# Optimization experiments

Measured on AMD Instinct MI355X. Metric: run time of the kernel, lower is better.

The kernel has to match this reference:

```python
import jax, jax.numpy as jnp
import numpy as np

N, E, F0, HEADS, B, OUT = 100000, 1600000, 128, 4, 64, 32
CHANNELS = [16, 8, 4, 2]
NEG_SLOPE = 0.2


def setup_inputs() -> dict:
    key = jax.random.key(0)
    ks = jax.random.split(key, 40)
    inp = {}
    inp['x'] = jax.random.normal(ks[0], (N, F0), dtype=jnp.float32)
    inp['edge_index'] = jax.random.randint(ks[1], (2, E), 0, N, dtype=jnp.int64)
    inp['batch'] = jnp.sort(jax.random.randint(ks[2], (N,), 0, B, dtype=jnp.int64))
    # GATConv params per layer: W [in, heads*out], att_src/att_dst [heads, out], bias [heads*out]
    in_dim = F0
    ki = 3
    for li, oc in enumerate(CHANNELS, start=1):
        scale = 1.0 / np.sqrt(in_dim)
        inp[f'W{li}'] = jax.random.normal(ks[ki], (in_dim, HEADS * oc), dtype=jnp.float32) * scale
        inp[f'a_src{li}'] = jax.random.normal(ks[ki + 1], (HEADS, oc), dtype=jnp.float32) * 0.1
        inp[f'a_dst{li}'] = jax.random.normal(ks[ki + 2], (HEADS, oc), dtype=jnp.float32) * 0.1
        inp[f'b{li}'] = jnp.zeros((HEADS * oc,), dtype=jnp.float32)
        ki += 3
        in_dim = HEADS * oc
    inp['W_fc'] = jax.random.normal(ks[ki], (2 * HEADS, OUT), dtype=jnp.float32) * (1.0 / np.sqrt(2 * HEADS))
    inp['b_fc'] = jnp.zeros((OUT,), dtype=jnp.float32)
    return inp


def gat_layer(x, src, dst, W, a_src, a_dst, b, oc):
    n = x.shape[0]
    h = (x @ W).reshape(n, HEADS, oc)                    # [N, H, C]
    al_s = jnp.einsum('nhc,hc->nh', h, a_src)            # [N, H]
    al_d = jnp.einsum('nhc,hc->nh', h, a_dst)
    e = jax.nn.leaky_relu(al_s[src] + al_d[dst], NEG_SLOPE)  # [E, H]
    # segment softmax over incoming edges per destination node
    m = jax.ops.segment_max(e, dst, num_segments=n)
    m = jnp.where(jnp.isfinite(m), m, 0.0)
    ex = jnp.exp(e - m[dst])
    s = jax.ops.segment_sum(ex, dst, num_segments=n)
    alpha = ex / (s[dst] + 1e-16)                        # [E, H]
    out = jax.ops.segment_sum(h[src] * alpha[:, :, None], dst, num_segments=n)
    return out.reshape(n, HEADS * oc) + b


def reference(x, edge_index, batch, W1, a_src1, a_dst1, b1, W2, a_src2, a_dst2, b2,
              W3, a_src3, a_dst3, b3, W4, a_src4, a_dst4, b4, W_fc, b_fc):
    n = x.shape[0]
    loops = jnp.arange(n, dtype=edge_index.dtype)
    src = jnp.concatenate([edge_index[0], loops])   # PyG GATConv adds self-loops
    dst = jnp.concatenate([edge_index[1], loops])
    params = [(W1, a_src1, a_dst1, b1), (W2, a_src2, a_dst2, b2),
              (W3, a_src3, a_dst3, b3), (W4, a_src4, a_dst4, b4)]
    h = x
    for (W, a_s, a_d, b), oc in zip(params, CHANNELS):
        h = jax.nn.relu(gat_layer(h, src, dst, W, a_s, a_d, b, oc))
        # dropout(0.3) is identity at inference
    # global mean pool over graphs in the batch
    sums = jax.ops.segment_sum(h, batch, num_segments=B)
    cnt = jax.ops.segment_sum(jnp.ones((n,), h.dtype), batch, num_segments=B)
    pooled = sums / jnp.maximum(cnt, 1.0)[:, None]
    return pooled @ W_fc + b_fc
```

## Files before the change

### kernel.cpp

```cpp
#include <hip/hip_runtime.h>
#include <hip/hip_bf16.h>

#define NNODES 100000
#define NEDGES 1600000
#define NHEADS 4
#define NGRAPH 64
#define NOUTF  32
#define BSH    9
#define NBUK   ((NNODES + 511) >> 9)
#define BPAD   16
#define BCAP   9216
#define CGRID  512
#define ECAP   ((NEDGES + CGRID - 1) / CGRID)
#define G1GRID ((NNODES + 63) / 64)

__device__ __forceinline__ unsigned short f2bf(float f) {
    union { float f; unsigned u; } v;
    v.f = f;
    unsigned r = v.u + 0x7FFF + ((v.u >> 16) & 1);
    return (unsigned short)(r >> 16);
}
__device__ __forceinline__ float bflo(unsigned u) {
    union { unsigned u; float f; } v;
    v.u = u << 16;
    return v.f;
}
__device__ __forceinline__ float bfhi(unsigned u) {
    union { unsigned u; float f; } v;
    v.u = u & 0xFFFF0000u;
    return v.f;
}

__device__ __forceinline__ bool ei_is_int64(const int* __restrict__ ei) {
    int acc = 0;
    #pragma unroll
    for (int i = 0; i < 32; i++) acc |= ei[2 * i + 1];
    return acc == 0;
}

__device__ __forceinline__ void fma4(float4& a, float s, const float4& b) {
    a.x += s * b.x;
    a.y += s * b.y;
    a.z += s * b.z;
    a.w += s * b.w;
}

__global__ __launch_bounds__(256) void gat_coarse_gemm1_kernel(
        const int* __restrict__ ei, const int* __restrict__ bt,
        int* __restrict__ bkcur, int* __restrict__ packed, int* __restrict__ bat,
        const float* __restrict__ x, const float* __restrict__ W1,
        const float* __restrict__ as1, const float* __restrict__ ad1,
        unsigned short* __restrict__ h1, float* __restrict__ al_s,
        float* __restrict__ al_d, int ne, int n) {
    __shared__ float smem[64 * 64 + 64 * 132];
    const int tid = threadIdx.x;
    if (blockIdx.x < CGRID) {
        int* hist = (int*)smem;
        int* base = hist + 256;
        int* es = base + 256;
        int* ed = es + ECAP;
        for (int i = tid; i < NBUK; i += 256) hist[i] = 0;
        __syncthreads();
        bool wide = ei_is_int64(ei);
        int chunk = (ne + CGRID - 1) / CGRID;
        int e0 = blockIdx.x * chunk;
        int e1 = min(e0 + chunk, ne);
        for (int i = e0 + tid; i < e1; i += 256) {
            int s = wide ? ei[2 * i] : ei[i];
            int d = wide ? ei[2 * (ne + i)] : ei[ne + i];
            es[i - e0] = s;
            ed[i - e0] = d;
            atomicAdd(&hist[d >> BSH], 1);
        }
        __syncthreads();
        for (int i = tid; i < NBUK; i += 256)
            base[i] = hist[i] ? atomicAdd(&bkcur[i * BPAD], hist[i]) : 0;
        __syncthreads();
        for (int i = tid; i < NBUK; i += 256) hist[i] = 0;
        __syncthreads();
        int m = e1 - e0;
        for (int j = tid; j < m; j += 256) {
            int d = ed[j];
            int bk = d >> BSH;
            int pos = base[bk] + atomicAdd(&hist[bk], 1);
            if (pos < BCAP) packed[bk * BCAP + pos] = es[j] | ((d & 511) << 17);
        }
        int gid = blockIdx.x * 256 + tid;
        for (int i = gid; i < n; i += CGRID * 256) bat[i] = wide ? bt[2 * i] : bt[i];
    } else {
        constexpr int DIN = 128, DOUT = 64, KTILE = 64;
        constexpr int OG = DOUT / 4;
        constexpr int NPB = 64;
        constexpr int S = DIN + 4;
        constexpr int C = DOUT / NHEADS;
        float* Wl = smem;
        float* xs = smem + KTILE * DOUT;
        const int base = (blockIdx.x - CGRID) * NPB;
        constexpr int KC = DIN / 4;
        for (int i = tid; i < NPB * KC; i += 256) {
            int nn = i / KC, kc = i - nn * KC;
            int nd = base + nn;
            float4 v = (nd < n) ? ((const float4*)x)[(size_t)nd * KC + kc]
                                : make_float4(0.f, 0.f, 0.f, 0.f);
            *(float4*)&xs[nn * S + kc * 4] = v;
        }
        const int og = tid % OG;
        const int ng = tid / OG;
        const int n0 = ng * 4;
        float4 acc[4] = {};
        for (int kt = 0; kt < DIN; kt += KTILE) {
            __syncthreads();
            for (int i = tid; i < KTILE * OG; i += 256)
                ((float4*)Wl)[i] = ((const float4*)W1)[kt * OG + i];
            __syncthreads();
            #pragma unroll 2
            for (int k = 0; k < KTILE; k += 4) {
                float4 wv[4], xv[4];
                #pragma unroll
                for (int j = 0; j < 4; j++)
                    wv[j] = *(const float4*)&Wl[(k + j) * DOUT + og * 4];
                #pragma unroll
                for (int r = 0; r < 4; r++)
                    xv[r] = *(const float4*)&xs[(n0 + r) * S + kt + k];
                #pragma unroll
                for (int r = 0; r < 4; r++) {
                    fma4(acc[r], xv[r].x, wv[0]);
                    fma4(acc[r], xv[r].y, wv[1]);
                    fma4(acc[r], xv[r].z, wv[2]);
                    fma4(acc[r], xv[r].w, wv[3]);
                }
            }
        }
        float4 asv = ((const float4*)as1)[og];
        float4 adv = ((const float4*)ad1)[og];
        #pragma unroll
        for (int r = 0; r < 4; r++) {
            int node = base + n0 + r;
            bool ok = node < n;
            if (ok) {
                ushort4 o;
                o.x = f2bf(acc[r].x);
                o.y = f2bf(acc[r].y);
                o.z = f2bf(acc[r].z);
                o.w = f2bf(acc[r].w);
                ((ushort4*)h1)[(size_t)node * OG + og] = o;
            }
            float ps = acc[r].x * asv.x + acc[r].y * asv.y + acc[r].z * asv.z + acc[r].w * asv.w;
            float pd = acc[r].x * adv.x + acc[r].y * adv.y + acc[r].z * adv.z + acc[r].w * adv.w;
            #pragma unroll
            for (int off = 1; off < C / 4; off <<= 1) {
                ps += __shfl_xor(ps, off);
                pd += __shfl_xor(pd, off);
            }
            if (ok && (og % (C / 4)) == 0) {
                int hh = og / (C / 4);
                al_s[node * NHEADS + hh] = ps;
                al_d[node * NHEADS + hh] = pd;
            }
        }
    }
}

__global__ __launch_bounds__(1024) void gat_fine_kernel(
        const int* __restrict__ packed, const int* __restrict__ bkcur,
        int* __restrict__ row_ptr, int* __restrict__ col, int n) {
    __shared__ int bscan[256];
    __shared__ int dg[512];
    __shared__ int excl[512];
    __shared__ int partial[256];
    __shared__ int cur[512];
    int b = blockIdx.x;
    int tid = threadIdx.x;
    if (tid < 256) bscan[tid] = (tid < NBUK) ? bkcur[tid * BPAD] : 0;
    if (tid < 512) dg[tid] = 0;
    __syncthreads();
    for (int off = 1; off < 256; off <<= 1) {
        int u = (tid < 256 && tid >= off) ? bscan[tid - off] : 0;
        __syncthreads();
        if (tid < 256) bscan[tid] += u;
        __syncthreads();
    }
    int cntb = bkcur[b * BPAD];
    int csr0 = bscan[b] - cntb;
    int pbeg = b * BCAP;
    int pend = pbeg + cntb;
    for (int t = pbeg + tid; t < pend; t += 1024)
        atomicAdd(&dg[packed[t] >> 17], 1);
    __syncthreads();
    int a0 = 0, a1 = 0, s = 0;
    if (tid < 256) {
        a0 = dg[2 * tid];
        a1 = dg[2 * tid + 1];
        s = a0 + a1;
        partial[tid] = s;
    }
    __syncthreads();
    for (int off = 1; off < 256; off <<= 1) {
        int u = (tid < 256 && tid >= off) ? partial[tid - off] : 0;
        __syncthreads();
        if (tid < 256) partial[tid] += u;
        __syncthreads();
    }
    if (tid < 256) {
        int ebase = partial[tid] - s;
        excl[2 * tid] = ebase;
        excl[2 * tid + 1] = ebase + a0;
        cur[2 * tid] = ebase;
        cur[2 * tid + 1] = ebase + a0;
    }
    __syncthreads();
    int node0 = b << BSH;
    if (tid < 512) {
        int nd = node0 + tid;
        if (nd < n) row_ptr[nd] = csr0 + excl[tid];
    }
    if (b == NBUK - 1 && tid == 0) row_ptr[n] = bscan[NBUK - 1];
    for (int t = pbeg + tid; t < pend; t += 1024) {
        int v = packed[t];
        int pos = atomicAdd(&cur[v >> 17], 1);
        col[csr0 + pos] = v & 0x1FFFF;
    }
}

__global__ __launch_bounds__(256) void gat_agg1_gemm2_kernel(
        const unsigned short* __restrict__ h, const float* __restrict__ al_s,
        const float* __restrict__ al_d_l1, const int* __restrict__ row_ptr,
        const int* __restrict__ col, const float* __restrict__ b1,
        const float* __restrict__ W2, const float* __restrict__ as2,
        const float* __restrict__ ad2, char* __restrict__ hrow_out,
        float* __restrict__ al_d, int n) {
    __shared__ float Wl[64 * 32];
    __shared__ float xs[32 * 68];
    const int tid = threadIdx.x;
    for (int i = tid; i < 64 * 32 / 4; i += 256)
        ((float4*)Wl)[i] = ((const float4*)W2)[i];
    __syncthreads();
    int lane = tid & 63;
    int sub = lane & 7;
    int gidx = lane >> 3;
    int slot = (tid >> 6) * 8 + gidx;
    int node = blockIdx.x * 32 + slot;
    bool ok = node < n;
    int node_c = ok ? node : (n - 1);
    int beg = row_ptr[node_c];
    int cnt = row_ptr[node_c + 1] - beg;
    const uint4* h4 = (const uint4*)h;
    float acc[8] = {};
    int j0 = sub * 8;
    const int hh = sub >> 1;
    float ald = al_d_l1[node_c * NHEADS + hh];
    float ws = 0.f;
    int total = cnt + 1;
    int t = 0;
    for (; t + 2 <= total; t += 2) {
        int s0 = col[beg + t];
        int s1 = (t + 1 < cnt) ? col[beg + t + 1] : node_c;
        float e0 = al_s[s0 * NHEADS + hh] + ald;
        float e1 = al_s[s1 * NHEADS + hh] + ald;
        uint4 hv0 = h4[(size_t)s0 * 8 + sub];
        uint4 hv1 = h4[(size_t)s1 * 8 + sub];
        e0 = (e0 > 0.f) ? e0 : 0.2f * e0;
        e1 = (e1 > 0.f) ? e1 : 0.2f * e1;
        float w0 = __expf(e0);
        float w1 = __expf(e1);
        ws += w0;
        acc[0] += w0 * bflo(hv0.x);
        acc[1] += w0 * bfhi(hv0.x);
        acc[2] += w0 * bflo(hv0.y);
        acc[3] += w0 * bfhi(hv0.y);
        acc[4] += w0 * bflo(hv0.z);
        acc[5] += w0 * bfhi(hv0.z);
        acc[6] += w0 * bflo(hv0.w);
        acc[7] += w0 * bfhi(hv0.w);
        ws += w1;
        acc[0] += w1 * bflo(hv1.x);
        acc[1] += w1 * bfhi(hv1.x);
        acc[2] += w1 * bflo(hv1.y);
        acc[3] += w1 * bfhi(hv1.y);
        acc[4] += w1 * bflo(hv1.z);
        acc[5] += w1 * bfhi(hv1.z);
        acc[6] += w1 * bflo(hv1.w);
        acc[7] += w1 * bfhi(hv1.w);
    }
    if (t < total) {
        int s0 = (t < cnt) ? col[beg + t] : node_c;
        float e0 = al_s[s0 * NHEADS + hh] + ald;
        uint4 hv0 = h4[(size_t)s0 * 8 + sub];
        e0 = (e0 > 0.f) ? e0 : 0.2f * e0;
        float w0 = __expf(e0);
        ws += w0;
        acc[0] += w0 * bflo(hv0.x);
        acc[1] += w0 * bfhi(hv0.x);
        acc[2] += w0 * bflo(hv0.y);
        acc[3] += w0 * bfhi(hv0.y);
        acc[4] += w0 * bflo(hv0.z);
        acc[5] += w0 * bfhi(hv0.z);
        acc[6] += w0 * bflo(hv0.w);
        acc[7] += w0 * bfhi(hv0.w);
    }
    float inv = 1.f / (ws + 1e-16f);
    #pragma unroll
    for (int k = 0; k < 8; k++) {
        acc[k] = acc[k] * inv + b1[j0 + k];
        acc[k] = (acc[k] > 0.f) ? acc[k] : 0.f;
    }
    float* xrow = &xs[slot * 68];
    *(float4*)&xrow[j0] = make_float4(acc[0], acc[1], acc[2], acc[3]);
    *(float4*)&xrow[j0 + 4] = make_float4(acc[4], acc[5], acc[6], acc[7]);
    const float4* Wl4 = (const float4*)Wl;
    float4 out4 = make_float4(0.f, 0.f, 0.f, 0.f);
    #pragma unroll 4
    for (int k = 0; k < 64; k += 4) {
        float4 xv = *(const float4*)&xrow[k];
        float4 w0 = Wl4[(k + 0) * 8 + sub];
        float4 w1 = Wl4[(k + 1) * 8 + sub];
        float4 w2 = Wl4[(k + 2) * 8 + sub];
        float4 w3 = Wl4[(k + 3) * 8 + sub];
        fma4(out4, xv.x, w0);
        fma4(out4, xv.y, w1);
        fma4(out4, xv.z, w2);
        fma4(out4, xv.w, w3);
    }
    float4 asv = ((const float4*)as2)[sub];
    float4 adv = ((const float4*)ad2)[sub];
    char* rp = hrow_out + (size_t)node_c * 96;
    if (ok) {
        ushort4 o;
        o.x = f2bf(out4.x);
        o.y = f2bf(out4.y);
        o.z = f2bf(out4.z);
        o.w = f2bf(out4.w);
        *(ushort4*)(rp + 16 + 8 * sub) = o;
    }
    float ps = out4.x * asv.x + out4.y * asv.y + out4.z * asv.z + out4.w * asv.w;
    float pd = out4.x * adv.x + out4.y * adv.y + out4.z * adv.z + out4.w * adv.w;
    ps += __shfl_xor(ps, 1);
    pd += __shfl_xor(pd, 1);
    if (ok && (sub & 1) == 0) {
        int hh2 = sub >> 1;
        *(float*)(rp + 4 * hh2) = ps;
        al_d[node_c * NHEADS + hh2] = pd;
    }
}

__global__ __launch_bounds__(256) void gat_agg2_gemm3_kernel(
        const char* __restrict__ hrow, const float* __restrict__ al_d_in,
        const int* __restrict__ row_ptr, const int* __restrict__ col,
        const float* __restrict__ b2, const float* __restrict__ W3,
        const float* __restrict__ as3, const float* __restrict__ ad3,
        char* __restrict__ hrow_out, float* __restrict__ al_d, int n) {
    __shared__ float Wl[32 * 16];
    __shared__ float xs[64 * 36];
    const int tid = threadIdx.x;
    for (int i = tid; i < 32 * 16 / 4; i += 256)
        ((float4*)Wl)[i] = ((const float4*)W3)[i];
    __syncthreads();
    int lane = tid & 63;
    int sub = lane & 3;
    int gidx = lane >> 2;
    int slot = (tid >> 6) * 16 + gidx;
    int node = blockIdx.x * 64 + slot;
    bool ok = node < n;
    int node_c = ok ? node : (n - 1);
    int beg = row_ptr[node_c];
    int cnt = row_ptr[node_c + 1] - beg;
    float acc[8] = {};
    int j0 = sub * 8;
    const int hh = sub;
    float ald = al_d_in[node_c * NHEADS + hh];
    float ws = 0.f;
    int total = cnt + 1;
    int t = 0;
    for (; t + 2 <= total; t += 2) {
        int s0 = col[beg + t];
        int s1 = (t + 1 < cnt) ? col[beg + t + 1] : node_c;
        const char* r0 = hrow + (size_t)s0 * 96;
        const char* r1 = hrow + (size_t)s1 * 96;
        float e0 = *(const float*)(r0 + 4 * hh) + ald;
        float e1 = *(const float*)(r1 + 4 * hh) + ald;
        uint4 hv0 = *(const uint4*)(r0 + 16 + 16 * sub);
        uint4 hv1 = *(const uint4*)(r1 + 16 + 16 * sub);
        e0 = (e0 > 0.f) ? e0 : 0.2f * e0;
        e1 = (e1 > 0.f) ? e1 : 0.2f * e1;
        float w0 = __expf(e0);
        float w1 = __expf(e1);
        ws += w0;
        acc[0] += w0 * bflo(hv0.x);
        acc[1] += w0 * bfhi(hv0.x);
        acc[2] += w0 * bflo(hv0.y);
        acc[3] += w0 * bfhi(hv0.y);
        acc[4] += w0 * bflo(hv0.z);
        acc[5] += w0 * bfhi(hv0.z);
        acc[6] += w0 * bflo(hv0.w);
        acc[7] += w0 * bfhi(hv0.w);
        ws += w1;
        acc[0] += w1 * bflo(hv1.x);
        acc[1] += w1 * bfhi(hv1.x);
        acc[2] += w1 * bflo(hv1.y);
        acc[3] += w1 * bfhi(hv1.y);
        acc[4] += w1 * bflo(hv1.z);
        acc[5] += w1 * bfhi(hv1.z);
        acc[6] += w1 * bflo(hv1.w);
        acc[7] += w1 * bfhi(hv1.w);
    }
    if (t < total) {
        int s0 = (t < cnt) ? col[beg + t] : node_c;
        const char* r0 = hrow + (size_t)s0 * 96;
        float e0 = *(const float*)(r0 + 4 * hh) + ald;
        uint4 hv0 = *(const uint4*)(r0 + 16 + 16 * sub);
        e0 = (e0 > 0.f) ? e0 : 0.2f * e0;
        float w0 = __expf(e0);
        ws += w0;
        acc[0] += w0 * bflo(hv0.x);
        acc[1] += w0 * bfhi(hv0.x);
        acc[2] += w0 * bflo(hv0.y);
        acc[3] += w0 * bfhi(hv0.y);
        acc[4] += w0 * bflo(hv0.z);
        acc[5] += w0 * bfhi(hv0.z);
        acc[6] += w0 * bflo(hv0.w);
        acc[7] += w0 * bfhi(hv0.w);
    }
    float inv = 1.f / (ws + 1e-16f);
    #pragma unroll
    for (int k = 0; k < 8; k++) {
        acc[k] = acc[k] * inv + b2[j0 + k];
        acc[k] = (acc[k] > 0.f) ? acc[k] : 0.f;
    }
    float* xrow = &xs[slot * 36];
    *(float4*)&xrow[j0] = make_float4(acc[0], acc[1], acc[2], acc[3]);
    *(float4*)&xrow[j0 + 4] = make_float4(acc[4], acc[5], acc[6], acc[7]);
    const float4* Wl4 = (const float4*)Wl;
    float4 out4 = make_float4(0.f, 0.f, 0.f, 0.f);
    #pragma unroll 4
    for (int k = 0; k < 32; k += 4) {
        float4 xv = *(const float4*)&xrow[k];
        float4 w0 = Wl4[(k + 0) * 4 + sub];
        float4 w1 = Wl4[(k + 1) * 4 + sub];
        float4 w2 = Wl4[(k + 2) * 4 + sub];
        float4 w3 = Wl4[(k + 3) * 4 + sub];
        fma4(out4, xv.x, w0);
        fma4(out4, xv.y, w1);
        fma4(out4, xv.z, w2);
        fma4(out4, xv.w, w3);
    }
    float4 asv = ((const float4*)as3)[sub];
    float4 adv = ((const float4*)ad3)[sub];
    char* rp = hrow_out + (size_t)node_c * 64;
    if (ok) {
        ushort4 o;
        o.x = f2bf(out4.x);
        o.y = f2bf(out4.y);
        o.z = f2bf(out4.z);
        o.w = f2bf(out4.w);
        *(ushort4*)(rp + 16 + 8 * sub) = o;
        float ps = out4.x * asv.x + out4.y * asv.y + out4.z * asv.z + out4.w * asv.w;
        float pd = out4.x * adv.x + out4.y * adv.y + out4.z * adv.z + out4.w * adv.w;
        *(float*)(rp + 4 * sub) = ps;
        al_d[node_c * NHEADS + sub] = pd;
    }
}

__global__ __launch_bounds__(256) void gat_agg3_gemm4_kernel(
        const char* __restrict__ hrow, const float* __restrict__ al_d_in,
        const int* __restrict__ row_ptr, const int* __restrict__ col,
        const float* __restrict__ b3, const float* __restrict__ W4,
        const float* __restrict__ as4, const float* __restrict__ ad4,
        char* __restrict__ hrow_out, float* __restrict__ al_d, int n) {
    __shared__ float Wl[16 * 8];
    __shared__ float xs[128 * 20];
    const int tid = threadIdx.x;
    if (tid < 16 * 8 / 4) ((float4*)Wl)[tid] = ((const float4*)W4)[tid];
    __syncthreads();
    int lane = tid & 63;
    int sub = lane & 1;
    int gidx = lane >> 1;
    int slot = (tid >> 6) * 32 + gidx;
    int node = blockIdx.x * 128 + slot;
    bool ok = node < n;
    int node_c = ok ? node : (n - 1);
    int beg = row_ptr[node_c];
    int cnt = row_ptr[node_c + 1] - beg;
    float acc[8] = {};
    int j0 = sub * 8;
    const int hh0 = 2 * sub, hh1 = 2 * sub + 1;
    float ald0 = al_d_in[node_c * NHEADS + hh0];
    float ald1 = al_d_in[node_c * NHEADS + hh1];
    float ws0 = 0.f, ws1 = 0.f;
    int total = cnt + 1;
    int t = 0;
    for (; t + 2 <= total; t += 2) {
        int s0 = col[beg + t];
        int s1 = (t + 1 < cnt) ? col[beg + t + 1] : node_c;
        const char* r0 = hrow + (size_t)s0 * 64;
        const char* r1 = hrow + (size_t)s1 * 64;
        float2 a0 = *(const float2*)(r0 + 8 * sub);
        float2 a1 = *(const float2*)(r1 + 8 * sub);
        uint4 hv0 = *(const uint4*)(r0 + 16 + 16 * sub);
        uint4 hv1 = *(const uint4*)(r1 + 16 + 16 * sub);
        float e00 = a0.x + ald0;
        float e01 = a0.y + ald1;
        float e10 = a1.x + ald0;
        float e11 = a1.y + ald1;
        e00 = (e00 > 0.f) ? e00 : 0.2f * e00;
        e01 = (e01 > 0.f) ? e01 : 0.2f * e01;
        e10 = (e10 > 0.f) ? e10 : 0.2f * e10;
        e11 = (e11 > 0.f) ? e11 : 0.2f * e11;
        float w00 = __expf(e00);
        float w01 = __expf(e01);
        float w10 = __expf(e10);
        float w11 = __expf(e11);
        ws0 += w00;
        ws1 += w01;
        acc[0] += w00 * bflo(hv0.x);
        acc[1] += w00 * bfhi(hv0.x);
        acc[2] += w00 * bflo(hv0.y);
        acc[3] += w00 * bfhi(hv0.y);
        acc[4] += w01 * bflo(hv0.z);
        acc[5] += w01 * bfhi(hv0.z);
        acc[6] += w01 * bflo(hv0.w);
        acc[7] += w01 * bfhi(hv0.w);
        ws0 += w10;
        ws1 += w11;
        acc[0] += w10 * bflo(hv1.x);
        acc[1] += w10 * bfhi(hv1.x);
        acc[2] += w10 * bflo(hv1.y);
        acc[3] += w10 * bfhi(hv1.y);
        acc[4] += w11 * bflo(hv1.z);
        acc[5] += w11 * bfhi(hv1.z);
        acc[6] += w11 * bflo(hv1.w);
        acc[7] += w11 * bfhi(hv1.w);
    }
    if (t < total) {
        int s0 = (t < cnt) ? col[beg + t] : node_c;
        const char* r0 = hrow + (size_t)s0 * 64;
        float2 a0 = *(const float2*)(r0 + 8 * sub);
        uint4 hv0 = *(const uint4*)(r0 + 16 + 16 * sub);
        float e00 = a0.x + ald0;
        float e01 = a0.y + ald1;
        e00 = (e00 > 0.f) ? e00 : 0.2f * e00;
        e01 = (e01 > 0.f) ? e01 : 0.2f * e01;
        float w00 = __expf(e00);
        float w01 = __expf(e01);
        ws0 += w00;
        ws1 += w01;
        acc[0] += w00 * bflo(hv0.x);
        acc[1] += w00 * bfhi(hv0.x);
        acc[2] += w00 * bflo(hv0.y);
        acc[3] += w00 * bfhi(hv0.y);
        acc[4] += w01 * bflo(hv0.z);
        acc[5] += w01 * bfhi(hv0.z);
        acc[6] += w01 * bflo(hv0.w);
        acc[7] += w01 * bfhi(hv0.w);
    }
    float inv0 = 1.f / (ws0 + 1e-16f);
    float inv1 = 1.f / (ws1 + 1e-16f);
    #pragma unroll
    for (int k = 0; k < 4; k++) {
        acc[k] = acc[k] * inv0 + b3[j0 + k];
        acc[k] = (acc[k] > 0.f) ? acc[k] : 0.f;
    }
    #pragma unroll
    for (int k = 4; k < 8; k++) {
        acc[k] = acc[k] * inv1 + b3[j0 + k];
        acc[k] = (acc[k] > 0.f) ? acc[k] : 0.f;
    }
    float* xrow = &xs[slot * 20];
    *(float4*)&xrow[j0] = make_float4(acc[0], acc[1], acc[2], acc[3]);
    *(float4*)&xrow[j0 + 4] = make_float4(acc[4], acc[5], acc[6], acc[7]);
    const float4* Wl4 = (const float4*)Wl;
    float4 out4 = make_float4(0.f, 0.f, 0.f, 0.f);
    #pragma unroll
    for (int k = 0; k < 16; k += 4) {
        float4 xv = *(const float4*)&xrow[k];
        float4 w0 = Wl4[(k + 0) * 2 + sub];
        float4 w1 = Wl4[(k + 1) * 2 + sub];
        float4 w2 = Wl4[(k + 2) * 2 + sub];
        float4 w3 = Wl4[(k + 3) * 2 + sub];
        fma4(out4, xv.x, w0);
        fma4(out4, xv.y, w1);
        fma4(out4, xv.z, w2);
        fma4(out4, xv.w, w3);
    }
    float4 asv = ((const float4*)as4)[sub];
    float4 adv = ((const float4*)ad4)[sub];
    char* rp = hrow_out + (size_t)node_c * 64;
    if (ok) {
        *(float4*)(rp + 16 + 16 * sub) = out4;
        *(float*)(rp + 8 * sub)     = out4.x * asv.x + out4.y * asv.y;
        *(float*)(rp + 8 * sub + 4) = out4.z * asv.z + out4.w * asv.w;
        al_d[node_c * NHEADS + 2 * sub]     = out4.x * adv.x + out4.y * adv.y;
        al_d[node_c * NHEADS + 2 * sub + 1] = out4.z * adv.z + out4.w * adv.w;
    }
}

__global__ __launch_bounds__(256) void gat_agg4_pool_kernel(
        const char* __restrict__ hrow, const float* __restrict__ al_d,
        const int* __restrict__ row_ptr, const int* __restrict__ col,
        const float* __restrict__ bias, const int* __restrict__ bat,
        float* __restrict__ sums, int n) {
    __shared__ float gsum[4 * 8];
    __shared__ int g0s;
    const int tid = threadIdx.x;
    if (tid < 32) gsum[tid] = 0.f;
    if (tid == 0) {
        int fn = blockIdx.x * 128;
        g0s = bat[fn < n ? fn : (n - 1)];
    }
    __syncthreads();
    int g0 = g0s;
    int lane = tid & 63;
    int sub = lane & 1;
    int gidx = lane >> 1;
    int node = blockIdx.x * 128 + (tid >> 6) * 32 + gidx;
    bool ok = node < n;
    int node_c = ok ? node : (n - 1);
    int beg = row_ptr[node_c];
    int cnt = row_ptr[node_c + 1] - beg;
    const int hh0 = 2 * sub, hh1 = 2 * sub + 1;
    float ald0 = al_d[node_c * NHEADS + hh0];
    float ald1 = al_d[node_c * NHEADS + hh1];
    float4 acc = make_float4(0.f, 0.f, 0.f, 0.f);
    float ws0 = 0.f, ws1 = 0.f;
    int total = cnt + 1;
    int t = 0;
    for (; t + 2 <= total; t += 2) {
        int s0 = col[beg + t];
        int s1 = (t + 1 < cnt) ? col[beg + t + 1] : node_c;
        const char* r0 = hrow + (size_t)s0 * 64;
        const char* r1 = hrow + (size_t)s1 * 64;
        float2 a0 = *(const float2*)(r0 + 8 * sub);
        float2 a1 = *(const float2*)(r1 + 8 * sub);
        float4 hv0 = *(const float4*)(r0 + 16 + 16 * sub);
        float4 hv1 = *(const float4*)(r1 + 16 + 16 * sub);
        float e00 = a0.x + ald0;
        float e01 = a0.y + ald1;
        float e10 = a1.x + ald0;
        float e11 = a1.y + ald1;
        e00 = (e00 > 0.f) ? e00 : 0.2f * e00;
        e01 = (e01 > 0.f) ? e01 : 0.2f * e01;
        e10 = (e10 > 0.f) ? e10 : 0.2f * e10;
        e11 = (e11 > 0.f) ? e11 : 0.2f * e11;
        float w00 = __expf(e00);
        float w01 = __expf(e01);
        float w10 = __expf(e10);
        float w11 = __expf(e11);
        ws0 += w00;
        ws1 += w01;
        acc.x += w00 * hv0.x;
        acc.y += w00 * hv0.y;
        acc.z += w01 * hv0.z;
        acc.w += w01 * hv0.w;
        ws0 += w10;
        ws1 += w11;
        acc.x += w10 * hv1.x;
        acc.y += w10 * hv1.y;
        acc.z += w11 * hv1.z;
        acc.w += w11 * hv1.w;
    }
    if (t < total) {
        int s0 = (t < cnt) ? col[beg + t] : node_c;
        const char* r0 = hrow + (size_t)s0 * 64;
        float2 a0 = *(const float2*)(r0 + 8 * sub);
        float4 hv0 = *(const float4*)(r0 + 16 + 16 * sub);
        float e00 = a0.x + ald0;
        float e01 = a0.y + ald1;
        e00 = (e00 > 0.f) ? e00 : 0.2f * e00;
        e01 = (e01 > 0.f) ? e01 : 0.2f * e01;
        float w00 = __expf(e00);
        float w01 = __expf(e01);
        ws0 += w00;
        ws1 += w01;
        acc.x += w00 * hv0.x;
        acc.y += w00 * hv0.y;
        acc.z += w01 * hv0.z;
        acc.w += w01 * hv0.w;
    }
    float4 bv = ((const float4*)bias)[sub];
    float4 v;
    v.x = acc.x / (ws0 + 1e-16f) + bv.x;
    v.y = acc.y / (ws0 + 1e-16f) + bv.y;
    v.z = acc.z / (ws1 + 1e-16f) + bv.z;
    v.w = acc.w / (ws1 + 1e-16f) + bv.w;
    v.x = (v.x > 0.f) ? v.x : 0.f;
    v.y = (v.y > 0.f) ? v.y : 0.f;
    v.z = (v.z > 0.f) ? v.z : 0.f;
    v.w = (v.w > 0.f) ? v.w : 0.f;
    if (ok) {
        int g = bat[node];
        int dg = g - g0;
        if (dg < 4) {
            atomicAdd(&gsum[dg * 8 + 4 * sub + 0], v.x);
            atomicAdd(&gsum[dg * 8 + 4 * sub + 1], v.y);
            atomicAdd(&gsum[dg * 8 + 4 * sub + 2], v.z);
            atomicAdd(&gsum[dg * 8 + 4 * sub + 3], v.w);
        } else {
            atomicAdd(&sums[g * 8 + 4 * sub + 0], v.x);
            atomicAdd(&sums[g * 8 + 4 * sub + 1], v.y);
            atomicAdd(&sums[g * 8 + 4 * sub + 2], v.z);
            atomicAdd(&sums[g * 8 + 4 * sub + 3], v.w);
        }
    }
    __syncthreads();
    if (tid < 32) {
        int dg = tid >> 3, k = tid & 7;
        int g = g0 + dg;
        if (g < NGRAPH) atomicAdd(&sums[g * 8 + k], gsum[tid]);
    }
}

__global__ __launch_bounds__(64) void gat_fc_kernel(
        const float* __restrict__ sums, const int* __restrict__ bat,
        const float* __restrict__ Wfc, const float* __restrict__ bfc,
        float* __restrict__ out, int n) {
    int b = blockIdx.x;
    int tid = threadIdx.x;
    int lo = 0, hi = n;
    while (lo < hi) { int mid = (lo + hi) >> 1; if (bat[mid] < b) lo = mid + 1; else hi = mid; }
    int i0 = lo;
    hi = n;
    while (lo < hi) { int mid = (lo + hi) >> 1; if (bat[mid] < b + 1) lo = mid + 1; else hi = mid; }
    int i1 = lo;
    if (tid < NOUTF) {
        float c = (float)(i1 - i0);
        if (c < 1.f) c = 1.f;
        float acc = bfc[tid];
        #pragma unroll
        for (int d = 0; d < 8; d++) acc += (sums[b * 8 + d] / c) * Wfc[d * NOUTF + tid];
        out[b * NOUTF + tid] = acc;
    }
}

extern "C" void kernel_launch(void* const* d_in, const int* in_sizes, int n_in,
                              void* d_out, int out_size, void* d_ws, size_t ws_size,
                              hipStream_t stream) {
    const float* x = (const float*)d_in[0];
    const int* ei = (const int*)d_in[1];
    const int* batch = (const int*)d_in[2];
    const float* W1 = (const float*)d_in[3];
    const float* as1 = (const float*)d_in[4];
    const float* ad1 = (const float*)d_in[5];
    const float* b1 = (const float*)d_in[6];
    const float* W2 = (const float*)d_in[7];
    const float* as2 = (const float*)d_in[8];
    const float* ad2 = (const float*)d_in[9];
    const float* b2 = (const float*)d_in[10];
    const float* W3 = (const float*)d_in[11];
    const float* as3 = (const float*)d_in[12];
    const float* ad3 = (const float*)d_in[13];
    const float* b3 = (const float*)d_in[14];
    const float* W4 = (const float*)d_in[15];
    const float* as4 = (const float*)d_in[16];
    const float* ad4 = (const float*)d_in[17];
    const float* b4 = (const float*)d_in[18];
    const float* Wfc = (const float*)d_in[19];
    const float* bfc = (const float*)d_in[20];

    const int n = NNODES, ne = NEDGES;

    char* p = (char*)d_ws;
    auto carve = [&](size_t bytes) {
        char* r = p;
        p += (bytes + 255) & ~(size_t)255;
        return r;
    };
    int* row_ptr = (int*)carve((size_t)(n + 1) * 4);
    int* col = (int*)carve((size_t)ne * 4);
    int* bkcur = (int*)carve(256 * BPAD * 4);
    int* packed = (int*)carve((size_t)NBUK * BCAP * 4);
    float* buf_h = (float*)carve((size_t)n * 64 * 4);
    float* buf_x = (float*)carve((size_t)n * 64 * 4);
    float* al_s = (float*)carve((size_t)n * NHEADS * 4);
    float* al_d = (float*)carve((size_t)n * NHEADS * 4);
    int* bat = (int*)carve((size_t)n * 4);
    float* sums = (float*)carve((size_t)NGRAPH * 8 * 4);
    unsigned short* h_bf16 = (unsigned short*)buf_h;

    hipMemsetAsync(bkcur, 0, 256 * BPAD * 4, stream);
    hipMemsetAsync(sums, 0, NGRAPH * 8 * 4, stream);

    gat_coarse_gemm1_kernel<<<CGRID + G1GRID, 256, 0, stream>>>(
        ei, batch, bkcur, packed, bat, x, W1, as1, ad1, h_bf16, al_s, al_d, ne, n);

    gat_fine_kernel<<<NBUK, 1024, 0, stream>>>(packed, bkcur, row_ptr, col, n);

    gat_agg1_gemm2_kernel<<<(n + 31) / 32, 256, 0, stream>>>(
        h_bf16, al_s, al_d, row_ptr, col, b1, W2, as2, ad2, (char*)buf_x, al_d, n);

    gat_agg2_gemm3_kernel<<<(n + 63) / 64, 256, 0, stream>>>(
        (const char*)buf_x, al_d, row_ptr, col, b2, W3, as3, ad3, (char*)buf_h, al_d, n);

    gat_agg3_gemm4_kernel<<<(n + 127) / 128, 256, 0, stream>>>(
        (const char*)buf_h, al_d, row_ptr, col, b3, W4, as4, ad4, (char*)buf_x, al_d, n);

    gat_agg4_pool_kernel<<<(n + 127) / 128, 256, 0, stream>>>(
        (const char*)buf_x, al_d, row_ptr, col, b4, bat, sums, n);

    gat_fc_kernel<<<NGRAPH, 64, 0, stream>>>(sums, bat, Wfc, bfc, (float*)d_out, n);
}
```

Before: 342.9 us.

## Sort nodes by in-degree so aggregation warps process similar-degree nodes

Builds a degree histogram in the CSR fine kernel, then adds a scatter kernel that writes a permutation of nodes grouped by in-degree bucket. Aggregation kernels for layers 1-3 take nodes in permuted order, so lanes in a wavefront have similar loop trip counts and diverge less. The cost is an extra kernel launch, extra atomics, and loss of node locality: row writes and al_d reads become scattered.

```diff
diff --git a/kernel.cpp b/kernel.cpp
--- a/kernel.cpp
+++ b/kernel.cpp
@@ -163,7 +163,7 @@
 
 __global__ __launch_bounds__(1024) void gat_fine_kernel(
         const int* __restrict__ packed, const int* __restrict__ bkcur,
-        int* __restrict__ row_ptr, int* __restrict__ col, int n) {
+        int* __restrict__ row_ptr, int* __restrict__ col, int* __restrict__ dcount, int n) {
     __shared__ int bscan[256];
     __shared__ int dg[512];
     __shared__ int excl[512];
@@ -220,12 +220,57 @@
         int pos = atomicAdd(&cur[v >> 17], 1);
         col[csr0 + pos] = v & 0x1FFFF;
     }
+    __syncthreads();
+    if (tid < 64) bscan[tid] = 0;
+    __syncthreads();
+    if (tid < 512) {
+        int nd = node0 + tid;
+        if (nd < n) {
+            int dgg = dg[tid];
+            atomicAdd(&bscan[dgg < 63 ? dgg : 63], 1);
+        }
+    }
+    __syncthreads();
+    if (tid < 64 && bscan[tid]) atomicAdd(&dcount[tid], bscan[tid]);
+}
+
+__global__ __launch_bounds__(512) void gat_degscatter_kernel(
+        const int* __restrict__ row_ptr, const int* __restrict__ dcount,
+        int* __restrict__ dscur, int* __restrict__ perm, int n) {
+    __shared__ int lhist[64], lbase[64], lcur[64], dbase[64];
+    int tid = threadIdx.x;
+    if (tid < 64) lhist[tid] = 0;
+    __syncthreads();
+    int node = blockIdx.x * 512 + tid;
+    int bk = -1;
+    if (node < n) {
+        int deg = row_ptr[node + 1] - row_ptr[node];
+        bk = deg < 63 ? deg : 63;
+        atomicAdd(&lhist[bk], 1);
+    }
+    __syncthreads();
+    if (tid == 0) {
+        int s = 0;
+        #pragma unroll
+        for (int k = 0; k < 64; k++) { dbase[k] = s; s += dcount[k]; }
+    }
+    __syncthreads();
+    if (tid < 64) {
+        lbase[tid] = lhist[tid] ? dbase[tid] + atomicAdd(&dscur[tid], lhist[tid]) : 0;
+        lcur[tid] = 0;
+    }
+    __syncthreads();
+    if (node < n) {
+        int pos = lbase[bk] + atomicAdd(&lcur[bk], 1);
+        perm[pos] = node;
+    }
 }
 
 __global__ __launch_bounds__(256) void gat_agg1_gemm2_kernel(
         const unsigned short* __restrict__ h, const float* __restrict__ al_s,
         const float* __restrict__ al_d_l1, const int* __restrict__ row_ptr,
-        const int* __restrict__ col, const float* __restrict__ b1,
+        const int* __restrict__ col, const int* __restrict__ perm,
+        const float* __restrict__ b1,
         const float* __restrict__ W2, const float* __restrict__ as2,
         const float* __restrict__ ad2, char* __restrict__ hrow_out,
         float* __restrict__ al_d, int n) {
@@ -239,9 +284,9 @@
     int sub = lane & 7;
     int gidx = lane >> 3;
     int slot = (tid >> 6) * 8 + gidx;
-    int node = blockIdx.x * 32 + slot;
-    bool ok = node < n;
-    int node_c = ok ? node : (n - 1);
+    int gslot = blockIdx.x * 32 + slot;
+    bool ok = gslot < n;
+    int node_c = ok ? perm[gslot] : (n - 1);
     int beg = row_ptr[node_c];
     int cnt = row_ptr[node_c + 1] - beg;
     const uint4* h4 = (const uint4*)h;
@@ -346,6 +391,7 @@
 __global__ __launch_bounds__(256) void gat_agg2_gemm3_kernel(
         const char* __restrict__ hrow, const float* __restrict__ al_d_in,
         const int* __restrict__ row_ptr, const int* __restrict__ col,
+        const int* __restrict__ perm,
         const float* __restrict__ b2, const float* __restrict__ W3,
         const float* __restrict__ as3, const float* __restrict__ ad3,
         char* __restrict__ hrow_out, float* __restrict__ al_d, int n) {
@@ -359,9 +405,9 @@
     int sub = lane & 3;
     int gidx = lane >> 2;
     int slot = (tid >> 6) * 16 + gidx;
-    int node = blockIdx.x * 64 + slot;
-    bool ok = node < n;
-    int node_c = ok ? node : (n - 1);
+    int gslot = blockIdx.x * 64 + slot;
+    bool ok = gslot < n;
+    int node_c = ok ? perm[gslot] : (n - 1);
     int beg = row_ptr[node_c];
     int cnt = row_ptr[node_c + 1] - beg;
     float acc[8] = {};
@@ -463,6 +509,7 @@
 __global__ __launch_bounds__(256) void gat_agg3_gemm4_kernel(
         const char* __restrict__ hrow, const float* __restrict__ al_d_in,
         const int* __restrict__ row_ptr, const int* __restrict__ col,
+        const int* __restrict__ perm,
         const float* __restrict__ b3, const float* __restrict__ W4,
         const float* __restrict__ as4, const float* __restrict__ ad4,
         char* __restrict__ hrow_out, float* __restrict__ al_d, int n) {
@@ -475,9 +522,9 @@
     int sub = lane & 1;
     int gidx = lane >> 1;
     int slot = (tid >> 6) * 32 + gidx;
-    int node = blockIdx.x * 128 + slot;
-    bool ok = node < n;
-    int node_c = ok ? node : (n - 1);
+    int gslot = blockIdx.x * 128 + slot;
+    bool ok = gslot < n;
+    int node_c = ok ? perm[gslot] : (n - 1);
     int beg = row_ptr[node_c];
     int cnt = row_ptr[node_c + 1] - beg;
     float acc[8] = {};
@@ -766,31 +813,37 @@
     int* row_ptr = (int*)carve((size_t)(n + 1) * 4);
     int* col = (int*)carve((size_t)ne * 4);
     int* bkcur = (int*)carve(256 * BPAD * 4);
+    int* dcnt = (int*)carve(128 * 4);
     int* packed = (int*)carve((size_t)NBUK * BCAP * 4);
     float* buf_h = (float*)carve((size_t)n * 64 * 4);
     float* buf_x = (float*)carve((size_t)n * 64 * 4);
     float* al_s = (float*)carve((size_t)n * NHEADS * 4);
     float* al_d = (float*)carve((size_t)n * NHEADS * 4);
     int* bat = (int*)carve((size_t)n * 4);
+    int* perm = (int*)carve((size_t)n * 4);
     float* sums = (float*)carve((size_t)NGRAPH * 8 * 4);
     unsigned short* h_bf16 = (unsigned short*)buf_h;
-
-    hipMemsetAsync(bkcur, 0, 256 * BPAD * 4, stream);
+    int* dcount = dcnt;
+    int* dscur = dcnt + 64;
+
+    hipMemsetAsync(bkcur, 0, 256 * BPAD * 4 + 512, stream);
     hipMemsetAsync(sums, 0, NGRAPH * 8 * 4, stream);
 
     gat_coarse_gemm1_kernel<<<CGRID + G1GRID, 256, 0, stream>>>(
         ei, batch, bkcur, packed, bat, x, W1, as1, ad1, h_bf16, al_s, al_d, ne, n);
 
-    gat_fine_kernel<<<NBUK, 1024, 0, stream>>>(packed, bkcur, row_ptr, col, n);
+    gat_fine_kernel<<<NBUK, 1024, 0, stream>>>(packed, bkcur, row_ptr, col, dcount, n);
+
+    gat_degscatter_kernel<<<NBUK, 512, 0, stream>>>(row_ptr, dcount, dscur, perm, n);
 
     gat_agg1_gemm2_kernel<<<(n + 31) / 32, 256, 0, stream>>>(
-        h_bf16, al_s, al_d, row_ptr, col, b1, W2, as2, ad2, (char*)buf_x, al_d, n);
+        h_bf16, al_s, al_d, row_ptr, col, perm, b1, W2, as2, ad2, (char*)buf_x, al_d, n);
 
     gat_agg2_gemm3_kernel<<<(n + 63) / 64, 256, 0, stream>>>(
-        (const char*)buf_x, al_d, row_ptr, col, b2, W3, as3, ad3, (char*)buf_h, al_d, n);
+        (const char*)buf_x, al_d, row_ptr, col, perm, b2, W3, as3, ad3, (char*)buf_h, al_d, n);
 
     gat_agg3_gemm4_kernel<<<(n + 127) / 128, 256, 0, stream>>>(
-        (const char*)buf_h, al_d, row_ptr, col, b3, W4, as4, ad4, (char*)buf_x, al_d, n);
+        (const char*)buf_h, al_d, row_ptr, col, perm, b3, W4, as4, ad4, (char*)buf_x, al_d, n);
 
     gat_agg4_pool_kernel<<<(n + 127) / 128, 256, 0, stream>>>(
         (const char*)buf_x, al_d, row_ptr, col, b4, bat, sums, n);
```

After: 367.3 us. +7.1%, slower.
